# Kernel optimization log

Hardware: AMD Instinct MI355X
Metric: run time of the kernel (lower is better)

The kernel has to match this reference:

```python
import jax, jax.numpy as jnp
import numpy as np

IN_DIM = 256
OUT_DIM = 256
NUM = 5        # grid_size
K = 3          # spline_order
GRID_RANGE = (-1.0, 1.0)


def extend_grid(grid, k_extend):
    # grid: (in_dim, num+1) -> (in_dim, num+1+2*k_extend)
    h = (grid[:, -1:] - grid[:, :1]) / (grid.shape[1] - 1)
    for _ in range(k_extend):
        grid = jnp.concatenate([grid[:, :1] - h, grid, grid[:, -1:] + h], axis=1)
    return grid


def b_spline_basis(x, grid, k):
    # x: (B, in_dim), grid: (in_dim, G). Cox-de Boor recursion, vectorized.
    x = x[:, :, None]                 # (B, in, 1)
    g = grid[None, :, :]              # (1, in, G)
    B = ((x >= g[:, :, :-1]) & (x < g[:, :, 1:])).astype(x.dtype)  # order 0
    for p in range(1, k + 1):
        left = (x - g[:, :, :-(p + 1)]) / (g[:, :, p:-1] - g[:, :, :-(p + 1)])
        right = (g[:, :, p + 1:] - x) / (g[:, :, p + 1:] - g[:, :, 1:-p])
        B = left * B[:, :, :-1] + right * B[:, :, 1:]
    return jnp.nan_to_num(B)          # (B, in, num+k)


def setup_inputs() -> dict:
    key = jax.random.key(0)
    kx, kc, kb, ks = jax.random.split(key, 4)
    x = jax.random.uniform(kx, (2048, IN_DIM), dtype=jnp.float32,
                           minval=GRID_RANGE[0], maxval=GRID_RANGE[1])
    base_grid = jnp.broadcast_to(
        jnp.linspace(GRID_RANGE[0], GRID_RANGE[1], NUM + 1, dtype=jnp.float32)[None, :],
        (IN_DIM, NUM + 1))
    grid = extend_grid(base_grid, K)                        # (in, num+1+2k)
    coef = 0.1 * jax.random.normal(kc, (IN_DIM, OUT_DIM, NUM + K), dtype=jnp.float32)
    scale_base = ((jax.random.uniform(kb, (IN_DIM, OUT_DIM), dtype=jnp.float32) * 2 - 1)
                  / np.sqrt(IN_DIM).astype(np.float32))
    scale_sp = jnp.ones((IN_DIM, OUT_DIM), dtype=jnp.float32)
    mask = jnp.ones((IN_DIM, OUT_DIM), dtype=jnp.float32)
    return {"x": x, "grid": grid, "coef": coef,
            "scale_base": scale_base, "scale_sp": scale_sp, "mask": mask}


def reference(x, grid, coef, scale_base, scale_sp, mask):
    base = jax.nn.silu(x)                                   # (B, in)
    B = b_spline_basis(x, grid, K)                          # (B, in, num+k)
    # coef2curve: (B, in, G) x (in, out, G) -> (B, in, out)
    y = jnp.einsum('big,iog->bio', B, coef)
    y = scale_base[None, :, :] * base[:, :, None] + scale_sp[None, :, :] * y
    y = mask[None, :, :] * y
    return jnp.sum(y, axis=1)                               # (B, out)
```

## Files before the change

kernel.cpp:

```cpp
#include <hip/hip_runtime.h>

#define BATCH 2048
#define IND   256
#define OUTD  256

typedef __attribute__((ext_vector_type(8))) short bf16x8;
typedef __attribute__((ext_vector_type(4))) float f32x4;

__device__ __forceinline__ ushort f2bf(float f) {
    uint u = __builtin_bit_cast(uint, f);
    u += 0x7fffu + ((u >> 16) & 1u);
    return (ushort)(u >> 16);
}
__device__ __forceinline__ uint pack2(float lo, float hi) {
    return (uint)f2bf(lo) | ((uint)f2bf(hi) << 16);
}

#define BIASOFF (1u << 20)
#define WS_NEED ((size_t)BIASOFF + 4096)

__device__ __forceinline__ uint4 feat_pack(float xv) {
    const float u = (xv + 1.0f) * 2.5f;
    float cif = floorf(u);
    cif = fminf(fmaxf(cif, 0.0f), 4.0f);
    const int ci = (int)cif;
    const float f = u - cif, mf = 1.0f - f;
    const float f2 = f * f, f3 = f2 * f;
    const float k6 = 1.0f / 6.0f;
    const float w0 = mf * mf * mf * k6;
    const float w1 = (3.0f * f3 - 6.0f * f2 + 4.0f) * k6;
    const float w3 = f3 * k6;
    const float w2 = 1.0f - w0 - w1 - w3;
    const float sg = __fdividef(xv, 1.0f + __expf(-xv));
    const float B0 = (ci == 0) ? w0 : 0.f;
    const float B1 = (ci == 1) ? w0 : (ci == 0) ? w1 : 0.f;
    const float B2 = (ci == 2) ? w0 : (ci == 1) ? w1 : (ci == 0) ? w2 : 0.f;
    const float B3 = (ci == 3) ? w0 : (ci == 2) ? w1 : (ci == 1) ? w2 : (ci == 0) ? w3 : 0.f;
    const float B4 = (ci == 4) ? w0 : (ci == 3) ? w1 : (ci == 2) ? w2 : (ci == 1) ? w3 : 0.f;
    const float B5 = (ci == 4) ? w1 : (ci == 3) ? w2 : (ci == 2) ? w3 : 0.f;
    const float B6 = (ci == 4) ? w2 : (ci == 3) ? w3 : 0.f;
    uint4 v;
    v.x = pack2(sg, B0); v.y = pack2(B1, B2);
    v.z = pack2(B3, B4); v.w = pack2(B5, B6);
    return v;
}

__global__ __launch_bounds__(256) void kan_wb(
    const float* __restrict__ coef, const float* __restrict__ sb,
    const float* __restrict__ ss, const float* __restrict__ mask,
    uint4* __restrict__ W, float* __restrict__ bias)
{
    const int bid = blockIdx.x, tid = threadIdx.x;
    __shared__ float part[32][8];
    if (bid < 256) {
        const int io = bid * OUTD + tid;
        const float m = mask[io], b = sb[io], sp = ss[io];
        const float4* cp = reinterpret_cast<const float4*>(coef + (size_t)io * 8);
        const float4 c0 = cp[0], c1 = cp[1];
        const float wb = m * b, wsp = m * sp;
        const float c7 = c1.w;
        uint4 w;
        w.x = pack2(wb,                wsp * (c0.x - c7));
        w.y = pack2(wsp * (c0.y - c7), wsp * (c0.z - c7));
        w.z = pack2(wsp * (c0.w - c7), wsp * (c1.x - c7));
        w.w = pack2(wsp * (c1.y - c7), wsp * (c1.z - c7));
        W[io] = w;
    } else {
        const int o0 = (bid - 256) * 8;
        const int ol = tid & 7, ig = tid >> 3;
        float s = 0.f;
#pragma unroll
        for (int ii = 0; ii < 8; ++ii) {
            const int i = ig * 8 + ii;
            const int io = i * OUTD + o0 + ol;
            s += mask[io] * ss[io] * coef[(size_t)io * 8 + 7];
        }
        part[ig][ol] = s;
        __syncthreads();
        if (tid < 8) {
            float acc = 0.f;
#pragma unroll
            for (int g2 = 0; g2 < 32; ++g2) acc += part[g2][tid];
            bias[o0 + tid] = acc;
        }
    }
}

__global__ __launch_bounds__(512, 4) void kan_fgemm(
    const float* __restrict__ x, const uint4* __restrict__ W,
    const float* __restrict__ bias, float* __restrict__ out)
{
    __shared__ float xs[32 * 256];
    __shared__ uint4 At[32 * 32];

    const int tid  = threadIdx.x;
    const int lane = tid & 63, wid = tid >> 6;
    const int nh = wid & 1, kq = wid >> 1;
    const int r = lane & 15, g = lane >> 4;
    const int bid = blockIdx.x;
    const int xcd = bid & 7;
    const int o0 = (xcd >> 1) * 64;
    const int b0 = ((bid >> 3) * 2 + (xcd & 1)) * 32;

    {
        const int row = tid >> 4, c0 = (tid & 15) * 4;
#pragma unroll
        for (int q2 = 0; q2 < 4; ++q2) {
            const float4 v = *reinterpret_cast<const float4*>(
                x + (size_t)(b0 + row) * IND + c0 + q2 * 64);
            *reinterpret_cast<float4*>(xs + row * 256 + c0 + q2 * 64) = v;
        }
    }

    const int frow = tid >> 5;
    const int fil  = tid & 31;

    f32x4 acc[2][2] = {};
    __syncthreads();

#pragma unroll
    for (int t = 0; t < 8; ++t) {
        const int i0 = t * 32;

        const uint4* pB = W + (size_t)(i0 + kq * 8 + g) * OUTD + o0 + nh * 32 + r;
        const bf16x8 b00 = *reinterpret_cast<const bf16x8*>(pB);
        const bf16x8 b01 = *reinterpret_cast<const bf16x8*>(pB + 16);
        const bf16x8 b10 = *reinterpret_cast<const bf16x8*>(pB + 4 * OUTD);
        const bf16x8 b11 = *reinterpret_cast<const bf16x8*>(pB + 4 * OUTD + 16);

        const uint4 f0 = feat_pack(xs[frow * 256 + i0 + fil]);
        const uint4 f1 = feat_pack(xs[(frow + 16) * 256 + i0 + fil]);

        __syncthreads();
        At[frow * 32 + (fil ^ (frow & 7))] = f0;
        At[(frow + 16) * 32 + (fil ^ ((frow + 16) & 7))] = f1;
        __syncthreads();

        const int s0 = kq * 8 + g;
        const int s1 = s0 + 4;
        const int ra0 = r, ra1 = 16 + r;
        const bf16x8 a00 = *reinterpret_cast<const bf16x8*>(At + ra0 * 32 + (s0 ^ (ra0 & 7)));
        const bf16x8 a10 = *reinterpret_cast<const bf16x8*>(At + ra1 * 32 + (s0 ^ (ra1 & 7)));
        const bf16x8 a01 = *reinterpret_cast<const bf16x8*>(At + ra0 * 32 + (s1 ^ (ra0 & 7)));
        const bf16x8 a11 = *reinterpret_cast<const bf16x8*>(At + ra1 * 32 + (s1 ^ (ra1 & 7)));

        acc[0][0] = __builtin_amdgcn_mfma_f32_16x16x32_bf16(a00, b00, acc[0][0], 0, 0, 0);
        acc[0][1] = __builtin_amdgcn_mfma_f32_16x16x32_bf16(a00, b01, acc[0][1], 0, 0, 0);
        acc[1][0] = __builtin_amdgcn_mfma_f32_16x16x32_bf16(a10, b00, acc[1][0], 0, 0, 0);
        acc[1][1] = __builtin_amdgcn_mfma_f32_16x16x32_bf16(a10, b01, acc[1][1], 0, 0, 0);
        acc[0][0] = __builtin_amdgcn_mfma_f32_16x16x32_bf16(a01, b10, acc[0][0], 0, 0, 0);
        acc[0][1] = __builtin_amdgcn_mfma_f32_16x16x32_bf16(a01, b11, acc[0][1], 0, 0, 0);
        acc[1][0] = __builtin_amdgcn_mfma_f32_16x16x32_bf16(a11, b10, acc[1][0], 0, 0, 0);
        acc[1][1] = __builtin_amdgcn_mfma_f32_16x16x32_bf16(a11, b11, acc[1][1], 0, 0, 0);
    }

    __syncthreads();
    float* red = xs;
    if (kq > 0) {
        float* dst = red + (size_t)(nh * 3 + kq - 1) * 1024;
#pragma unroll
        for (int mf = 0; mf < 2; ++mf)
#pragma unroll
            for (int nf = 0; nf < 2; ++nf)
                *reinterpret_cast<f32x4*>(dst + (mf * 2 + nf) * 256 + lane * 4) = acc[mf][nf];
    }
    __syncthreads();
    if (kq == 0) {
#pragma unroll
        for (int mf = 0; mf < 2; ++mf)
#pragma unroll
            for (int nf = 0; nf < 2; ++nf) {
                f32x4 s = acc[mf][nf];
                const int sl = (mf * 2 + nf) * 256 + lane * 4;
#pragma unroll
                for (int kk = 0; kk < 3; ++kk) {
                    const f32x4 v = *reinterpret_cast<const f32x4*>(
                        red + (size_t)(nh * 3 + kk) * 1024 + sl);
                    s.x += v.x; s.y += v.y; s.z += v.z; s.w += v.w;
                }
                const int col  = o0 + nh * 32 + nf * 16 + r;
                const int row0 = b0 + mf * 16 + g * 4;
                const float bv = bias[col];
#pragma unroll
                for (int e = 0; e < 4; ++e)
                    out[(size_t)(row0 + e) * OUTD + col] = s[e] + bv;
            }
    }
}

#define KPI  16
#define IPC  8
#define KC   (IPC * KPI)

__global__ __launch_bounds__(256, 2) void kan_mfma(
    const float* __restrict__ x, const float* __restrict__ coef,
    const float* __restrict__ scale_base, const float* __restrict__ scale_sp,
    const float* __restrict__ mask, float* __restrict__ out)
{
    const int tid = threadIdx.x;
    const int b0 = blockIdx.x * 32, o0 = blockIdx.y * 32;
    __shared__ uint Fa[32 * KC / 2];
    __shared__ uint Wt2[32 * KC / 2];
    for (int j = tid; j < 32 * KC / 2; j += 256) { Fa[j] = 0u; Wt2[j] = 0u; }
    const int lane = tid & 63, wid = tid >> 6;
    const int wmv = (wid >> 1) * 16, wnv = (wid & 1) * 16;
    f32x4 acc = {0.f, 0.f, 0.f, 0.f};
    const int fb = tid & 31, il = tid >> 5;
    for (int ic = 0; ic < IND / IPC; ++ic) {
        const int i = ic * IPC + il;
        __syncthreads();
        {
            const uint4 fp = feat_pack(x[(b0 + fb) * IND + i]);
            const int base = fb * (KC / 2) + il * (KPI / 2);
            const int sw = (fb & 7) << 2;
            Fa[(base + 0) ^ sw] = fp.x; Fa[(base + 1) ^ sw] = fp.y;
            Fa[(base + 2) ^ sw] = fp.z; Fa[(base + 3) ^ sw] = fp.w;
            ((ushort*)Fa)[2 * ((base + 4) ^ sw)] = 0;
        }
        {
            const int io = i * OUTD + o0 + fb;
            const float m = mask[io];
            const float wb = scale_base[io] * m, wsv = scale_sp[io] * m;
            const float4* cp = reinterpret_cast<const float4*>(coef + (size_t)io * 8);
            const float4 c0 = cp[0], c1 = cp[1];
            const float c7 = c1.w;
            const int base = fb * (KC / 2) + il * (KPI / 2);
            const int sw = (fb & 7) << 2;
            Wt2[(base + 0) ^ sw] = pack2(wb, wsv * (c0.x - c7));
            Wt2[(base + 1) ^ sw] = pack2(wsv * (c0.y - c7), wsv * (c0.z - c7));
            Wt2[(base + 2) ^ sw] = pack2(wsv * (c0.w - c7), wsv * (c1.x - c7));
            Wt2[(base + 3) ^ sw] = pack2(wsv * (c1.y - c7), wsv * (c1.z - c7));
            ((ushort*)Wt2)[2 * ((base + 4) ^ sw)] = 0;
        }
        __syncthreads();
        {
            const ushort* fs = (const ushort*)Fa;
            const ushort* wsd = (const ushort*)Wt2;
            const int ar = wmv + (lane & 15), br = wnv + (lane & 15);
            const int kg = (lane >> 4) * 8;
#pragma unroll
            for (int ksi = 0; ksi < 4; ++ksi) {
                const int ka = ksi * 32 + kg;
                const int ia = (ar * KC + ka) ^ ((ar & 7) << 3);
                const int ib = (br * KC + ka) ^ ((br & 7) << 3);
                bf16x8 a = *reinterpret_cast<const bf16x8*>(fs + ia);
                bf16x8 b = *reinterpret_cast<const bf16x8*>(wsd + ib);
                acc = __builtin_amdgcn_mfma_f32_16x16x32_bf16(a, b, acc, 0, 0, 0);
            }
        }
    }
    const int col = o0 + wnv + (lane & 15);
    const int row0 = b0 + wmv + ((lane >> 4) << 2);
    float bv = 0.f;
    for (int i = 0; i < IND; ++i) {
        const int io = i * OUTD + col;
        bv += mask[io] * scale_sp[io] * coef[(size_t)io * 8 + 7];
    }
#pragma unroll
    for (int rr = 0; rr < 4; ++rr)
        out[(size_t)(row0 + rr) * OUTD + col] = acc[rr] + bv;
}

extern "C" void kernel_launch(void* const* d_in, const int* in_sizes, int n_in,
                              void* d_out, int out_size, void* d_ws, size_t ws_size,
                              hipStream_t stream) {
    const float* x          = (const float*)d_in[0];
    const float* coef       = (const float*)d_in[2];
    const float* scale_base = (const float*)d_in[3];
    const float* scale_sp   = (const float*)d_in[4];
    const float* mask       = (const float*)d_in[5];
    float* out = (float*)d_out;

    if (ws_size >= WS_NEED) {
        uint4* W    = (uint4*)d_ws;
        float* bias = (float*)((char*)d_ws + BIASOFF);
        kan_wb<<<288, 256, 0, stream>>>(coef, scale_base, scale_sp, mask, W, bias);
        kan_fgemm<<<256, 512, 0, stream>>>(x, W, bias, out);
    } else {
        kan_mfma<<<dim3(BATCH / 32, OUTD / 32), 256, 0, stream>>>(
            x, coef, scale_base, scale_sp, mask, out);
    }
}
```

Baseline: 18.93 us.

## Halve fgemm output tile width to 32 columns and double grid to 512 blocks

Changes the fused GEMM block tile from 32x64 to 32x32 outputs. The two wave halves now split the M dimension instead of N, so each wave does 4 MFMAs per step instead of 8. The grid doubles to 512 blocks to raise parallelism across the CUs. The cost is that each block recomputes the B-spline feature packing for its 32 rows, so that work is duplicated across twice as many blocks. The XCD-aware block-to-tile mapping is also replaced by a simple linear mapping.

```diff
diff --git a/kernel.cpp b/kernel.cpp
--- a/kernel.cpp
+++ b/kernel.cpp
@@ -95,12 +95,11 @@
 
     const int tid  = threadIdx.x;
     const int lane = tid & 63, wid = tid >> 6;
-    const int nh = wid & 1, kq = wid >> 1;
+    const int mh = wid & 1, kq = wid >> 1;
     const int r = lane & 15, g = lane >> 4;
     const int bid = blockIdx.x;
-    const int xcd = bid & 7;
-    const int o0 = (xcd >> 1) * 64;
-    const int b0 = ((bid >> 3) * 2 + (xcd & 1)) * 32;
+    const int o0 = (bid & 7) * 32;
+    const int b0 = (bid >> 3) * 32;
 
     {
         const int row = tid >> 4, c0 = (tid & 15) * 4;
@@ -115,14 +114,14 @@
     const int frow = tid >> 5;
     const int fil  = tid & 31;
 
-    f32x4 acc[2][2] = {};
+    f32x4 acc[2] = {};
     __syncthreads();
 
 #pragma unroll
     for (int t = 0; t < 8; ++t) {
         const int i0 = t * 32;
 
-        const uint4* pB = W + (size_t)(i0 + kq * 8 + g) * OUTD + o0 + nh * 32 + r;
+        const uint4* pB = W + (size_t)(i0 + kq * 8 + g) * OUTD + o0 + r;
         const bf16x8 b00 = *reinterpret_cast<const bf16x8*>(pB);
         const bf16x8 b01 = *reinterpret_cast<const bf16x8*>(pB + 16);
         const bf16x8 b10 = *reinterpret_cast<const bf16x8*>(pB + 4 * OUTD);
@@ -136,55 +135,44 @@
         At[(frow + 16) * 32 + (fil ^ ((frow + 16) & 7))] = f1;
         __syncthreads();
 
-        const int s0 = kq * 8 + g;
-        const int s1 = s0 + 4;
-        const int ra0 = r, ra1 = 16 + r;
-        const bf16x8 a00 = *reinterpret_cast<const bf16x8*>(At + ra0 * 32 + (s0 ^ (ra0 & 7)));
-        const bf16x8 a10 = *reinterpret_cast<const bf16x8*>(At + ra1 * 32 + (s0 ^ (ra1 & 7)));
-        const bf16x8 a01 = *reinterpret_cast<const bf16x8*>(At + ra0 * 32 + (s1 ^ (ra0 & 7)));
-        const bf16x8 a11 = *reinterpret_cast<const bf16x8*>(At + ra1 * 32 + (s1 ^ (ra1 & 7)));
-
-        acc[0][0] = __builtin_amdgcn_mfma_f32_16x16x32_bf16(a00, b00, acc[0][0], 0, 0, 0);
-        acc[0][1] = __builtin_amdgcn_mfma_f32_16x16x32_bf16(a00, b01, acc[0][1], 0, 0, 0);
-        acc[1][0] = __builtin_amdgcn_mfma_f32_16x16x32_bf16(a10, b00, acc[1][0], 0, 0, 0);
-        acc[1][1] = __builtin_amdgcn_mfma_f32_16x16x32_bf16(a10, b01, acc[1][1], 0, 0, 0);
-        acc[0][0] = __builtin_amdgcn_mfma_f32_16x16x32_bf16(a01, b10, acc[0][0], 0, 0, 0);
-        acc[0][1] = __builtin_amdgcn_mfma_f32_16x16x32_bf16(a01, b11, acc[0][1], 0, 0, 0);
-        acc[1][0] = __builtin_amdgcn_mfma_f32_16x16x32_bf16(a11, b10, acc[1][0], 0, 0, 0);
-        acc[1][1] = __builtin_amdgcn_mfma_f32_16x16x32_bf16(a11, b11, acc[1][1], 0, 0, 0);
+        const int arow = mh * 16 + r;
+        const int s0 = kq * 8 + g, s1 = s0 + 4;
+        const bf16x8 a0 = *reinterpret_cast<const bf16x8*>(At + arow * 32 + (s0 ^ (arow & 7)));
+        const bf16x8 a1 = *reinterpret_cast<const bf16x8*>(At + arow * 32 + (s1 ^ (arow & 7)));
+
+        acc[0] = __builtin_amdgcn_mfma_f32_16x16x32_bf16(a0, b00, acc[0], 0, 0, 0);
+        acc[1] = __builtin_amdgcn_mfma_f32_16x16x32_bf16(a0, b01, acc[1], 0, 0, 0);
+        acc[0] = __builtin_amdgcn_mfma_f32_16x16x32_bf16(a1, b10, acc[0], 0, 0, 0);
+        acc[1] = __builtin_amdgcn_mfma_f32_16x16x32_bf16(a1, b11, acc[1], 0, 0, 0);
     }
 
     __syncthreads();
     float* red = xs;
     if (kq > 0) {
-        float* dst = red + (size_t)(nh * 3 + kq - 1) * 1024;
-#pragma unroll
-        for (int mf = 0; mf < 2; ++mf)
-#pragma unroll
-            for (int nf = 0; nf < 2; ++nf)
-                *reinterpret_cast<f32x4*>(dst + (mf * 2 + nf) * 256 + lane * 4) = acc[mf][nf];
+        float* dst = red + (size_t)(mh * 3 + kq - 1) * 512;
+#pragma unroll
+        for (int nf = 0; nf < 2; ++nf)
+            *reinterpret_cast<f32x4*>(dst + nf * 256 + lane * 4) = acc[nf];
     }
     __syncthreads();
     if (kq == 0) {
 #pragma unroll
-        for (int mf = 0; mf < 2; ++mf)
-#pragma unroll
-            for (int nf = 0; nf < 2; ++nf) {
-                f32x4 s = acc[mf][nf];
-                const int sl = (mf * 2 + nf) * 256 + lane * 4;
-#pragma unroll
-                for (int kk = 0; kk < 3; ++kk) {
-                    const f32x4 v = *reinterpret_cast<const f32x4*>(
-                        red + (size_t)(nh * 3 + kk) * 1024 + sl);
-                    s.x += v.x; s.y += v.y; s.z += v.z; s.w += v.w;
-                }
-                const int col  = o0 + nh * 32 + nf * 16 + r;
-                const int row0 = b0 + mf * 16 + g * 4;
-                const float bv = bias[col];
-#pragma unroll
-                for (int e = 0; e < 4; ++e)
-                    out[(size_t)(row0 + e) * OUTD + col] = s[e] + bv;
+        for (int nf = 0; nf < 2; ++nf) {
+            f32x4 s = acc[nf];
+            const int sl = nf * 256 + lane * 4;
+#pragma unroll
+            for (int kk = 0; kk < 3; ++kk) {
+                const f32x4 v = *reinterpret_cast<const f32x4*>(
+                    red + (size_t)(mh * 3 + kk) * 512 + sl);
+                s.x += v.x; s.y += v.y; s.z += v.z; s.w += v.w;
             }
+            const int col  = o0 + nf * 16 + r;
+            const int row0 = b0 + mh * 16 + g * 4;
+            const float bv = bias[col];
+#pragma unroll
+            for (int e = 0; e < 4; ++e)
+                out[(size_t)(row0 + e) * OUTD + col] = s[e] + bv;
+        }
     }
 }
 
@@ -275,7 +263,7 @@
         uint4* W    = (uint4*)d_ws;
         float* bias = (float*)((char*)d_ws + BIASOFF);
         kan_wb<<<288, 256, 0, stream>>>(coef, scale_base, scale_sp, mask, W, bias);
-        kan_fgemm<<<256, 512, 0, stream>>>(x, W, bias, out);
+        kan_fgemm<<<512, 512, 0, stream>>>(x, W, bias, out);
     } else {
         kan_mfma<<<dim3(BATCH / 32, OUTD / 32), 256, 0, stream>>>(
             x, coef, scale_base, scale_sp, mask, out);
```

Result: slower. 22.87 us (+20.8%).

## Retile feature GEMM to 64x32 blocks with streamed x prefetch

Applied to the files above, without the earlier changes.

Block tile changes from 32 batch rows × 64 outputs to 64 batch rows × 32 outputs, with the two wave halves splitting rows instead of columns. The up-front load of the full 32x256 x tile into shared memory is replaced by a 64x32 slab that is refilled each k-step through register prefetch. Features are now computed once per row for the full 32-wide output tile, and shared memory shrinks. Each block does twice the feature expansion per k-step and reads W with half the column reuse, and launch bounds drop to 2 blocks per CU.

```diff
diff --git a/kernel.cpp b/kernel.cpp
--- a/kernel.cpp
+++ b/kernel.cpp
@@ -86,63 +86,74 @@
     }
 }
 
-__global__ __launch_bounds__(512, 4) void kan_fgemm(
+__global__ __launch_bounds__(512, 2) void kan_fgemm(
     const float* __restrict__ x, const uint4* __restrict__ W,
     const float* __restrict__ bias, float* __restrict__ out)
 {
-    __shared__ float xs[32 * 256];
-    __shared__ uint4 At[32 * 32];
+    __shared__ float xs2[64 * 32];
+    __shared__ uint4 At[64 * 32];
 
     const int tid  = threadIdx.x;
     const int lane = tid & 63, wid = tid >> 6;
-    const int nh = wid & 1, kq = wid >> 1;
+    const int mh = wid & 1, kq = wid >> 1;
     const int r = lane & 15, g = lane >> 4;
     const int bid = blockIdx.x;
-    const int xcd = bid & 7;
-    const int o0 = (xcd >> 1) * 64;
-    const int b0 = ((bid >> 3) * 2 + (xcd & 1)) * 32;
-
-    {
-        const int row = tid >> 4, c0 = (tid & 15) * 4;
-#pragma unroll
-        for (int q2 = 0; q2 < 4; ++q2) {
-            const float4 v = *reinterpret_cast<const float4*>(
-                x + (size_t)(b0 + row) * IND + c0 + q2 * 64);
-            *reinterpret_cast<float4*>(xs + row * 256 + c0 + q2 * 64) = v;
-        }
-    }
+    const int o0 = (bid & 7) * 32;
+    const int b0 = (bid >> 3) * 64;
 
     const int frow = tid >> 5;
     const int fil  = tid & 31;
 
+#pragma unroll
+    for (int p = 0; p < 4; ++p)
+        xs2[(frow + 16 * p) * 32 + fil] = x[(size_t)(b0 + frow + 16 * p) * IND + fil];
+    __syncthreads();
+
     f32x4 acc[2][2] = {};
-    __syncthreads();
 
 #pragma unroll
     for (int t = 0; t < 8; ++t) {
         const int i0 = t * 32;
 
-        const uint4* pB = W + (size_t)(i0 + kq * 8 + g) * OUTD + o0 + nh * 32 + r;
+        const uint4* pB = W + (size_t)(i0 + kq * 8 + g) * OUTD + o0 + r;
         const bf16x8 b00 = *reinterpret_cast<const bf16x8*>(pB);
         const bf16x8 b01 = *reinterpret_cast<const bf16x8*>(pB + 16);
         const bf16x8 b10 = *reinterpret_cast<const bf16x8*>(pB + 4 * OUTD);
         const bf16x8 b11 = *reinterpret_cast<const bf16x8*>(pB + 4 * OUTD + 16);
 
-        const uint4 f0 = feat_pack(xs[frow * 256 + i0 + fil]);
-        const uint4 f1 = feat_pack(xs[(frow + 16) * 256 + i0 + fil]);
+        float xp0 = 0.f, xp1 = 0.f, xp2 = 0.f, xp3 = 0.f;
+        if (t < 7) {
+            const float* px = x + (size_t)(b0 + frow) * IND + i0 + 32 + fil;
+            xp0 = px[0];
+            xp1 = px[16 * IND];
+            xp2 = px[32 * IND];
+            xp3 = px[48 * IND];
+        }
+
+        const uint4 f0 = feat_pack(xs2[frow * 32 + fil]);
+        const uint4 f1 = feat_pack(xs2[(frow + 16) * 32 + fil]);
+        const uint4 f2 = feat_pack(xs2[(frow + 32) * 32 + fil]);
+        const uint4 f3 = feat_pack(xs2[(frow + 48) * 32 + fil]);
 
         __syncthreads();
         At[frow * 32 + (fil ^ (frow & 7))] = f0;
         At[(frow + 16) * 32 + (fil ^ ((frow + 16) & 7))] = f1;
-        __syncthreads();
-
-        const int s0 = kq * 8 + g;
-        const int s1 = s0 + 4;
-        const int ra0 = r, ra1 = 16 + r;
-        const bf16x8 a00 = *reinterpret_cast<const bf16x8*>(At + ra0 * 32 + (s0 ^ (ra0 & 7)));
-        const bf16x8 a10 = *reinterpret_cast<const bf16x8*>(At + ra1 * 32 + (s0 ^ (ra1 & 7)));
-        const bf16x8 a01 = *reinterpret_cast<const bf16x8*>(At + ra0 * 32 + (s1 ^ (ra0 & 7)));
-        const bf16x8 a11 = *reinterpret_cast<const bf16x8*>(At + ra1 * 32 + (s1 ^ (ra1 & 7)));
+        At[(frow + 32) * 32 + (fil ^ ((frow + 32) & 7))] = f2;
+        At[(frow + 48) * 32 + (fil ^ ((frow + 48) & 7))] = f3;
+        if (t < 7) {
+            xs2[frow * 32 + fil] = xp0;
+            xs2[(frow + 16) * 32 + fil] = xp1;
+            xs2[(frow + 32) * 32 + fil] = xp2;
+            xs2[(frow + 48) * 32 + fil] = xp3;
+        }
+        __syncthreads();
+
+        const int ar0 = mh * 32 + r, ar1 = ar0 + 16;
+        const int s0 = kq * 8 + g, s1 = s0 + 4;
+        const bf16x8 a00 = *reinterpret_cast<const bf16x8*>(At + ar0 * 32 + (s0 ^ (ar0 & 7)));
+        const bf16x8 a10 = *reinterpret_cast<const bf16x8*>(At + ar1 * 32 + (s0 ^ (ar1 & 7)));
+        const bf16x8 a01 = *reinterpret_cast<const bf16x8*>(At + ar0 * 32 + (s1 ^ (ar0 & 7)));
+        const bf16x8 a11 = *reinterpret_cast<const bf16x8*>(At + ar1 * 32 + (s1 ^ (ar1 & 7)));
 
         acc[0][0] = __builtin_amdgcn_mfma_f32_16x16x32_bf16(a00, b00, acc[0][0], 0, 0, 0);
         acc[0][1] = __builtin_amdgcn_mfma_f32_16x16x32_bf16(a00, b01, acc[0][1], 0, 0, 0);
@@ -155,9 +166,9 @@
     }
 
     __syncthreads();
-    float* red = xs;
+    float* red = (float*)At;
     if (kq > 0) {
-        float* dst = red + (size_t)(nh * 3 + kq - 1) * 1024;
+        float* dst = red + (size_t)(mh * 3 + kq - 1) * 1024;
 #pragma unroll
         for (int mf = 0; mf < 2; ++mf)
 #pragma unroll
@@ -175,11 +186,11 @@
 #pragma unroll
                 for (int kk = 0; kk < 3; ++kk) {
                     const f32x4 v = *reinterpret_cast<const f32x4*>(
-                        red + (size_t)(nh * 3 + kk) * 1024 + sl);
+                        red + (size_t)(mh * 3 + kk) * 1024 + sl);
                     s.x += v.x; s.y += v.y; s.z += v.z; s.w += v.w;
                 }
-                const int col  = o0 + nh * 32 + nf * 16 + r;
-                const int row0 = b0 + mf * 16 + g * 4;
+                const int col  = o0 + nf * 16 + r;
+                const int row0 = b0 + mh * 32 + mf * 16 + g * 4;
                 const float bv = bias[col];
 #pragma unroll
                 for (int e = 0; e < 4; ++e)
```

Result: slower. 25.89 us (+36.8%).
